# Performance work log

Hardware: AMD Instinct MI355X
Metric: run time of the kernel (lower is better)

The kernel has to match this reference:

```python
import jax, jax.numpy as jnp
import numpy as np

B, T, D, H, TW = 4, 2048, 2048, 8, 4
DH = D // H


def setup_inputs() -> dict:
    key = jax.random.key(0)
    ks = jax.random.split(key, 16)
    s = lambda k, shape, std: jax.random.normal(k, shape, dtype=jnp.float32) * std
    inp = {
        "x": jax.random.normal(ks[0], (B, T, D), dtype=jnp.float32),
        "segment_pos": jnp.tile(jnp.arange(T, dtype=jnp.int32), (B, 1)),
        # linear_y / linear_x: width -> lru_width, std = 1/sqrt(width)
        "Wy": s(ks[1], (D, D), (1.0 / D) ** 0.5),
        "by": jnp.zeros((D,), jnp.float32),
        "Wx": s(ks[2], (D, D), (1.0 / D) ** 0.5),
        "bx": jnp.zeros((D,), jnp.float32),
        # depthwise causal conv: [temporal_width, lru_width]
        "conv_w": s(ks[3], (TW, D), (1.0 / TW) ** 0.5),
        "conv_b": jnp.zeros((D,), jnp.float32),
        # RG-LRU block-diagonal gates: [H, D/H, D/H]
        "gx_w": s(ks[4], (H, DH, DH), (1.0 / DH) ** 0.5),
        "gx_b": jnp.zeros((H, DH), jnp.float32),
        "ga_w": s(ks[5], (H, DH, DH), (1.0 / DH) ** 0.5),
        "ga_b": jnp.zeros((H, DH), jnp.float32),
        # a_param: softplus(a_param) > 0 controls decay rate
        "a_param": jnp.log(jnp.exp(jax.random.uniform(ks[6], (D,), minval=0.3, maxval=0.9)) - 1.0 + 1e-6),
        # linear_out: lru_width -> width, std = 1/sqrt(lru_width)
        "Wout": s(ks[7], (D, D), (1.0 / D) ** 0.5),
        "bout": jnp.zeros((D,), jnp.float32),
    }
    return inp


def _causal_conv1d(x, w, b, segment_pos):
    # depthwise causal conv over time; contributions from other segments masked
    t = x.shape[1]
    acc = jnp.zeros_like(x)
    for i in range(TW):
        shift = TW - 1 - i  # input at t - shift, weighted by w[i]
        xs = x if shift == 0 else jnp.pad(x, ((0, 0), (shift, 0), (0, 0)))[:, :t]
        mask = (segment_pos >= shift)[..., None].astype(x.dtype)
        acc = acc + xs * mask * w[i]
    return acc + b


def _rg_lru(x, segment_pos, gx_w, gx_b, ga_w, ga_b, a_param):
    b, t, d = x.shape
    xr = x.reshape(b, t, H, DH)
    gate_x = jax.nn.sigmoid(jnp.einsum("bthi,hij->bthj", xr, gx_w) + gx_b).reshape(b, t, d)
    gate_a = jax.nn.sigmoid(jnp.einsum("bthi,hij->bthj", xr, ga_w) + ga_b).reshape(b, t, d)
    log_a = -8.0 * gate_a * jax.nn.softplus(a_param)  # [B,T,D]
    a = jnp.exp(log_a)
    reset = (segment_pos == 0)[..., None]  # [B,T,1]
    multiplier = jnp.sqrt(jnp.maximum(1.0 - jnp.exp(2.0 * log_a), 0.0))
    multiplier = jnp.where(reset, 1.0, multiplier)
    normed = x * gate_x * multiplier
    a_scan = jnp.where(reset, 0.0, a)

    def step(h, inputs):
        a_t, x_t = inputs
        h = a_t * h + x_t
        return h, h

    h0 = jnp.zeros((b, d), x.dtype)
    _, ys = jax.lax.scan(step, h0, (a_scan.transpose(1, 0, 2), normed.transpose(1, 0, 2)))
    return ys.transpose(1, 0, 2)


def reference(x, segment_pos, Wy, by, Wx, bx, conv_w, conv_b, gx_w, gx_b, ga_w, ga_b, a_param, Wout, bout):
    y = jax.nn.gelu(x @ Wy.T + by, approximate=True)
    x_proj = x @ Wx.T + bx
    x_conv = _causal_conv1d(x_proj, conv_w, conv_b, segment_pos)
    x_lru = _rg_lru(x_conv, segment_pos, gx_w, gx_b, ga_w, ga_b, a_param)
    out = (x_lru * y) @ Wout.T + bout
    return out
```

## Files before the change

kernel.cpp:

```cpp
#include <hip/hip_runtime.h>
#include <cstdint>
#include <cstddef>

typedef __bf16 bf16;
typedef __bf16 bf16x8 __attribute__((ext_vector_type(8)));
typedef float f32x4 __attribute__((ext_vector_type(4)));

#define BDIM 4
#define TDIM 2048
#define DDIM 2048
#define HDIM 8
#define DHD 256
#define MTOT 8192
#define NCHUNK 64
#define LCHUNK 32

__device__ __forceinline__ void stage16(const bf16* g, bf16* l) {
  __builtin_amdgcn_global_load_lds(
      (const __attribute__((address_space(1))) void*)g,
      (__attribute__((address_space(3))) void*)l, 16, 0, 0);
}

#define SBAR() asm volatile("s_barrier" ::: "memory")
#define WAITVM(N) asm volatile("s_waitcnt vmcnt(" #N ")" ::: "memory")

__device__ __forceinline__ float sigmoid_f(float x) {
  return __fdividef(1.f, 1.f + __expf(-x));
}
__device__ __forceinline__ float gelu_tanh(float v) {
  float u = 0.7978845608028654f * (v + 0.044715f * v * v * v);
  u = fminf(fmaxf(u, -15.f), 15.f);
  float t = __expf(2.f * u);
  return 0.5f * v * (1.f + __fdividef(t - 1.f, t + 1.f));
}
__device__ __forceinline__ float softplus_f(float x) {
  return __logf(1.f + __expf(x));
}

__global__ __launch_bounds__(256) void f2b(const float* __restrict__ src,
                                           bf16* __restrict__ dst) {
  size_t i = ((size_t)blockIdx.x * 256 + threadIdx.x) * 8;
  const float4 a = *(const float4*)(src + i);
  const float4 b = *(const float4*)(src + i + 4);
  bf16x8 r;
  r[0] = (bf16)a.x; r[1] = (bf16)a.y; r[2] = (bf16)a.z; r[3] = (bf16)a.w;
  r[4] = (bf16)b.x; r[5] = (bf16)b.y; r[6] = (bf16)b.z; r[7] = (bf16)b.w;
  *(bf16x8*)(dst + i) = r;
}

template <typename TO, int EPI>
__global__ __launch_bounds__(512, 2) void gemm256(
    const bf16* __restrict__ A, const bf16* __restrict__ Bm,
    const float* __restrict__ bias, TO* __restrict__ C,
    int K, int lda, int ldb, int ldc) {
  const int n0 = blockIdx.x * 256;
  const int m0 = blockIdx.y * 256;
  __shared__ bf16 sA[2][256][64];
  __shared__ bf16 sB[2][256][64];
  const int tid = threadIdx.x;
  const int lane = tid & 63;
  const int wid = tid >> 6;
  const int wr = wid >> 2;
  const int wc = wid & 3;
  const int quad = lane >> 4;
  const int l15 = lane & 15;

  const int sr = tid >> 3;
  const int ks8 = ((tid & 7) ^ (sr & 7)) << 3;
  const bf16* Ag = A + (size_t)(m0 + sr) * lda + ks8;
  const bf16* Bg = Bm + (size_t)(n0 + sr) * ldb + ks8;

  const int swz0 = ((quad) ^ (l15 & 7)) << 3;
  const int swz1 = ((4 + quad) ^ (l15 & 7)) << 3;

  f32x4 acc[8][4];
#pragma unroll
  for (int i = 0; i < 8; ++i)
#pragma unroll
    for (int j = 0; j < 4; ++j)
#pragma unroll
      for (int r = 0; r < 4; ++r) acc[i][j][r] = 0.f;

  const int NT = K >> 6;

  auto STAGE = [&](int p, int tk) {
    const size_t ko = (size_t)tk << 6;
#pragma unroll
    for (int c = 0; c < 4; ++c) {
      stage16(Ag + (size_t)(c * 64) * lda + ko, &sA[p][c * 64 + wid * 8][0]);
      stage16(Bg + (size_t)(c * 64) * ldb + ko, &sB[p][c * 64 + wid * 8][0]);
    }
  };

  STAGE(0, 0);
  STAGE(1, 1);
  WAITVM(8);
  SBAR();

  int p = 0;
  for (int t = 0; t < NT; ++t) {
    const bf16* As0 = &sA[p][0][0];
    const bf16* Bs0 = &sB[p][0][0];
#pragma unroll
    for (int mh = 0; mh < 2; ++mh) {
      bf16x8 afr[4][2];
#pragma unroll
      for (int mi = 0; mi < 4; ++mi) {
        const int arow = wr * 128 + mh * 64 + mi * 16 + l15;
        afr[mi][0] = *(const bf16x8*)(As0 + arow * 64 + swz0);
        afr[mi][1] = *(const bf16x8*)(As0 + arow * 64 + swz1);
      }
#pragma unroll
      for (int nh = 0; nh < 2; ++nh) {
        bf16x8 bfr[2][2];
#pragma unroll
        for (int ni = 0; ni < 2; ++ni) {
          const int brow = wc * 64 + nh * 32 + ni * 16 + l15;
          bfr[ni][0] = *(const bf16x8*)(Bs0 + brow * 64 + swz0);
          bfr[ni][1] = *(const bf16x8*)(Bs0 + brow * 64 + swz1);
        }
        __builtin_amdgcn_s_setprio(1);
#pragma unroll
        for (int mi = 0; mi < 4; ++mi)
#pragma unroll
          for (int ni = 0; ni < 2; ++ni) {
            acc[mh * 4 + mi][nh * 2 + ni] = __builtin_amdgcn_mfma_f32_16x16x32_bf16(
                afr[mi][0], bfr[ni][0], acc[mh * 4 + mi][nh * 2 + ni], 0, 0, 0);
            acc[mh * 4 + mi][nh * 2 + ni] = __builtin_amdgcn_mfma_f32_16x16x32_bf16(
                afr[mi][1], bfr[ni][1], acc[mh * 4 + mi][nh * 2 + ni], 0, 0, 0);
          }
        __builtin_amdgcn_s_setprio(0);
      }
    }
    SBAR();
    if (t + 2 < NT) {
      STAGE(p, t + 2);
      WAITVM(8);
    } else {
      WAITVM(0);
    }
    SBAR();
    p ^= 1;
  }

#pragma unroll
  for (int nn = 0; nn < 4; ++nn) {
    const int n = n0 + wc * 64 + nn * 16 + l15;
    const float bv = bias[n];
#pragma unroll
    for (int mm = 0; mm < 8; ++mm) {
#pragma unroll
      for (int r = 0; r < 4; ++r) {
        const int m = m0 + wr * 128 + mm * 16 + quad * 4 + r;
        float v = acc[mm][nn][r] + bv;
        if (EPI == 1) v = gelu_tanh(v);
        C[(size_t)m * ldc + n] = (TO)v;
      }
    }
  }
}

__global__ __launch_bounds__(256) void gate_gemm(
    const bf16* __restrict__ xconv,
    const bf16* __restrict__ gxT, const bf16* __restrict__ gaT,
    bf16* __restrict__ gxr, bf16* __restrict__ gar) {
  const int h = blockIdx.z >> 1;
  const int g = blockIdx.z & 1;
  const bf16* A = xconv + h * DHD;
  const bf16* Bm = (g ? gaT : gxT) + (size_t)h * DHD * DHD;
  bf16* C = (g ? gar : gxr) + h * DHD;
  const int n0 = blockIdx.x * 128;
  const int m0 = blockIdx.y * 128;
  __shared__ bf16 As[128 * 32];
  __shared__ bf16 Bs[128 * 32];
  const int tid = threadIdx.x;
  const int lane = tid & 63;
  const int wid = tid >> 6;
  const int waveM = wid >> 1, waveN = wid & 1;
  const int quad = lane >> 4;
  const int l15 = lane & 15;
  const int srow = lane >> 2;
  const int scol = (lane & 3) * 8;

  f32x4 acc[4][4];
#pragma unroll
  for (int i = 0; i < 4; ++i)
#pragma unroll
    for (int j = 0; j < 4; ++j)
#pragma unroll
      for (int r = 0; r < 4; ++r) acc[i][j][r] = 0.f;

  for (int k0 = 0; k0 < DHD; k0 += 32) {
    if (k0) __syncthreads();
#pragma unroll
    for (int cc = 0; cc < 2; ++cc) {
      const int q = wid * 2 + cc;
      const int row = q * 16 + srow;
      stage16(A + (size_t)(m0 + row) * DDIM + k0 + scol, As + q * 512);
      stage16(Bm + (size_t)(n0 + row) * DHD + k0 + scol, Bs + q * 512);
    }
    __syncthreads();
    bf16x8 af[4], bfr[4];
#pragma unroll
    for (int i = 0; i < 4; ++i) {
      af[i]  = *(const bf16x8*)&As[(waveM * 64 + i * 16 + l15) * 32 + quad * 8];
      bfr[i] = *(const bf16x8*)&Bs[(waveN * 64 + i * 16 + l15) * 32 + quad * 8];
    }
#pragma unroll
    for (int i = 0; i < 4; ++i)
#pragma unroll
      for (int j = 0; j < 4; ++j)
        acc[i][j] = __builtin_amdgcn_mfma_f32_16x16x32_bf16(af[i], bfr[j], acc[i][j], 0, 0, 0);
  }

#pragma unroll
  for (int j = 0; j < 4; ++j) {
    const int n = n0 + waveN * 64 + j * 16 + l15;
#pragma unroll
    for (int i = 0; i < 4; ++i) {
#pragma unroll
      for (int r = 0; r < 4; ++r) {
        const int m = m0 + waveM * 64 + i * 16 + quad * 4 + r;
        C[(size_t)m * DDIM + n] = (bf16)acc[i][j][r];
      }
    }
  }
}

__global__ __launch_bounds__(256) void conv_kernel(
    const bf16* __restrict__ xp, const float* __restrict__ cw,
    const float* __restrict__ cb, const int* __restrict__ segp,
    bf16* __restrict__ xc) {
  int v = blockIdx.x * 256 + threadIdx.x;
  int dv = v & (DDIM / 8 - 1);
  int m = v >> 8;
  int d0 = dv * 8;
  int t = m & (TDIM - 1);
  int sp = segp[m];
  float acc[8];
#pragma unroll
  for (int j = 0; j < 8; ++j) acc[j] = cb[d0 + j];
#pragma unroll
  for (int i = 0; i < 4; ++i) {
    int shift = 3 - i;
    if (t >= shift && sp >= shift) {
      bf16x8 xv = *(const bf16x8*)&xp[(size_t)(m - shift) * DDIM + d0];
#pragma unroll
      for (int j = 0; j < 8; ++j) acc[j] = fmaf((float)xv[j], cw[i * DDIM + d0 + j], acc[j]);
    }
  }
  bf16x8 o;
#pragma unroll
  for (int j = 0; j < 8; ++j) o[j] = (bf16)acc[j];
  *(bf16x8*)&xc[(size_t)m * DDIM + d0] = o;
}

__global__ __launch_bounds__(256) void transpose_gates(
    const float* __restrict__ gxw, const float* __restrict__ gaw,
    bf16* __restrict__ gxT, bf16* __restrict__ gaT) {
  __shared__ bf16 tile[32][33];
  int zz = blockIdx.z;
  int h = zz >> 1;
  const float* src = (zz & 1) ? gaw : gxw;
  bf16* dst = (zz & 1) ? gaT : gxT;
  int j0 = blockIdx.x * 32;
  int i0 = blockIdx.y * 32;
  int r = threadIdx.x >> 5;
  int c = threadIdx.x & 31;
  for (int rr = r; rr < 32; rr += 8)
    tile[rr][c] = (bf16)src[(size_t)(h * DHD + i0 + rr) * DHD + j0 + c];
  __syncthreads();
  for (int rr = r; rr < 32; rr += 8)
    dst[(size_t)(h * DHD + j0 + rr) * DHD + i0 + c] = tile[c][rr];
}

__device__ __forceinline__ void lru_elem(float pgx, float pga, float xc,
                                         float spv, bool reset,
                                         float& a, float& nr) {
  const float gx = sigmoid_f(pgx);
  const float ga = sigmoid_f(pga);
  const float la = -8.f * ga * spv;
  a = reset ? 0.f : __expf(la);
  const float mult = reset ? 1.f : sqrtf(fmaxf(1.f - __expf(2.f * la), 0.f));
  nr = xc * gx * mult;
}

__global__ __launch_bounds__(256) void scan_phase1(
    const bf16* __restrict__ gxr, const bf16* __restrict__ gar,
    const bf16* __restrict__ xconv,
    const float* __restrict__ gxb, const float* __restrict__ gab,
    const float* __restrict__ apar, const int* __restrict__ segp,
    float* __restrict__ chA, float* __restrict__ chH) {
  int idx = blockIdx.x * 256 + threadIdx.x;
  int d = idx & (DDIM - 1);
  int c = (idx >> 11) & (NCHUNK - 1);
  int b = idx >> 17;
  const float gxbv = gxb[d], gabv = gab[d];
  const float spv = softplus_f(apar[d]);
  const int mrow = b * TDIM + c * LCHUNK;
  size_t base = (size_t)mrow * DDIM + d;
  float A = 1.f, hh = 0.f;
  for (int i = 0; i < LCHUNK; ++i) {
    size_t o = base + (size_t)i * DDIM;
    float a, nr;
    lru_elem((float)gxr[o] + gxbv, (float)gar[o] + gabv, (float)xconv[o],
             spv, segp[mrow + i] == 0, a, nr);
    hh = fmaf(a, hh, nr);
    A *= a;
  }
  int ci = (b * NCHUNK + c) * DDIM + d;
  chA[ci] = A;
  chH[ci] = hh;
}

__global__ __launch_bounds__(256) void scan_phase2(
    const float* __restrict__ chA, const float* __restrict__ chH,
    float* __restrict__ hst) {
  int idx = blockIdx.x * 256 + threadIdx.x;
  int d = idx & (DDIM - 1);
  int b = idx >> 11;
  float s = 0.f;
  for (int c = 0; c < NCHUNK; ++c) {
    int ci = (b * NCHUNK + c) * DDIM + d;
    hst[ci] = s;
    s = fmaf(chA[ci], s, chH[ci]);
  }
}

__global__ __launch_bounds__(256) void scan_phase3(
    const bf16* __restrict__ gxr, const bf16* __restrict__ gar,
    const bf16* __restrict__ xconv,
    const float* __restrict__ gxb, const float* __restrict__ gab,
    const float* __restrict__ apar, const int* __restrict__ segp,
    const float* __restrict__ hst, bf16* __restrict__ yz) {
  int idx = blockIdx.x * 256 + threadIdx.x;
  int d = idx & (DDIM - 1);
  int c = (idx >> 11) & (NCHUNK - 1);
  int b = idx >> 17;
  const float gxbv = gxb[d], gabv = gab[d];
  const float spv = softplus_f(apar[d]);
  const int mrow = b * TDIM + c * LCHUNK;
  size_t base = (size_t)mrow * DDIM + d;
  float hh = hst[(b * NCHUNK + c) * DDIM + d];
  for (int i = 0; i < LCHUNK; ++i) {
    size_t o = base + (size_t)i * DDIM;
    float a, nr;
    lru_elem((float)gxr[o] + gxbv, (float)gar[o] + gabv, (float)xconv[o],
             spv, segp[mrow + i] == 0, a, nr);
    hh = fmaf(a, hh, nr);
    yz[o] = (bf16)(hh * (float)yz[o]);
  }
}

extern "C" void kernel_launch(void* const* d_in, const int* in_sizes, int n_in,
                              void* d_out, int out_size, void* d_ws, size_t ws_size,
                              hipStream_t stream) {
  const float* x    = (const float*)d_in[0];
  const int*   segp = (const int*)d_in[1];
  const float* Wy   = (const float*)d_in[2];
  const float* by   = (const float*)d_in[3];
  const float* Wx   = (const float*)d_in[4];
  const float* bx   = (const float*)d_in[5];
  const float* cw   = (const float*)d_in[6];
  const float* cb   = (const float*)d_in[7];
  const float* gxw  = (const float*)d_in[8];
  const float* gxb  = (const float*)d_in[9];
  const float* gaw  = (const float*)d_in[10];
  const float* gab  = (const float*)d_in[11];
  const float* apar = (const float*)d_in[12];
  const float* Wout = (const float*)d_in[13];
  const float* bout = (const float*)d_in[14];

  const size_t MD = (size_t)MTOT * DDIM;
  const size_t WD = (size_t)DDIM * DDIM;
  bf16* xb    = (bf16*)d_out;
  bf16* xproj = (bf16*)((char*)d_out + MD * 2);
  bf16* xconv = xb;
  bf16* gxr   = xproj;

  char* ws = (char*)d_ws;
  bf16*  gar = (bf16*)ws;
  bf16*  W1  = (bf16*)(ws + MD * 2);
  bf16*  WB1 = (bf16*)(ws + 2 * MD * 2);
  bf16*  WB2 = (bf16*)(ws + 2 * MD * 2 + WD * 2);
  char*  tail = ws + 2 * MD * 2 + 2 * WD * 2;
  const size_t GW = (size_t)HDIM * DHD * DHD * 2;
  const size_t CH = (size_t)BDIM * NCHUNK * DDIM * 4;
  bf16*  gxT = (bf16*)tail;
  bf16*  gaT = (bf16*)(tail + GW);
  float* chA = (float*)(tail + 2 * GW);
  float* chH = (float*)(tail + 2 * GW + CH);
  float* hst = (float*)(tail + 2 * GW + 2 * CH);

  dim3 blk(256);
  f2b<<<dim3(MD / 2048), blk, 0, stream>>>(x, xb);
  f2b<<<dim3(WD / 2048), blk, 0, stream>>>(Wx, WB1);
  f2b<<<dim3(WD / 2048), blk, 0, stream>>>(Wy, WB2);
  transpose_gates<<<dim3(8, 8, 16), blk, 0, stream>>>(gxw, gaw, gxT, gaT);

  gemm256<bf16, 0><<<dim3(8, 32), dim3(512), 0, stream>>>(xb, WB1, bx, xproj, DDIM, DDIM, DDIM, DDIM);
  gemm256<bf16, 1><<<dim3(8, 32), dim3(512), 0, stream>>>(xb, WB2, by, W1, DDIM, DDIM, DDIM, DDIM);

  conv_kernel<<<dim3(MTOT * (DDIM / 8) / 256), blk, 0, stream>>>(xproj, cw, cb, segp, xconv);

  gate_gemm<<<dim3(2, 64, 16), blk, 0, stream>>>(xconv, gxT, gaT, gxr, gar);

  scan_phase1<<<dim3(BDIM * NCHUNK * DDIM / 256), blk, 0, stream>>>(
      gxr, gar, xconv, gxb, gab, apar, segp, chA, chH);
  scan_phase2<<<dim3(BDIM * DDIM / 256), blk, 0, stream>>>(chA, chH, hst);
  scan_phase3<<<dim3(BDIM * NCHUNK * DDIM / 256), blk, 0, stream>>>(
      gxr, gar, xconv, gxb, gab, apar, segp, hst, W1);

  f2b<<<dim3(WD / 2048), blk, 0, stream>>>(Wout, WB1);
  gemm256<float, 0><<<dim3(8, 32), dim3(512), 0, stream>>>(W1, WB1, bout, (float*)d_out, DDIM, DDIM, DDIM, DDIM);
}
```

Before: 452.4 us.

## Interleave LDS reads, global staging and MFMA clusters in GEMM main loop; remap workgroups

Restructures the GEMM main loop into four MFMA quadrants, with LDS fragment reads and global-to-LDS staging of the next tile spread between them under extra barriers, so memory traffic overlaps with matrix math. The loop-end wait-and-barrier pair becomes a single wait at the top of each iteration. It also remaps workgroup IDs in chunks of eight, intended to improve L2/XCD locality across the grid. In exchange there are more barriers per iteration and higher register pressure from holding all A and B fragments. The early overwrite of the current buffer relies on every fragment already having been read into registers.

Measured after the change: 420.5 us. 7.1% less time.

```diff
diff --git a/kernel.cpp b/kernel.cpp
--- a/kernel.cpp
+++ b/kernel.cpp
@@ -23,6 +23,7 @@
 
 #define SBAR() asm volatile("s_barrier" ::: "memory")
 #define WAITVM(N) asm volatile("s_waitcnt vmcnt(" #N ")" ::: "memory")
+#define LGKM0() asm volatile("s_waitcnt lgkmcnt(0)" ::: "memory")
 
 __device__ __forceinline__ float sigmoid_f(float x) {
   return __fdividef(1.f, 1.f + __expf(-x));
@@ -53,8 +54,14 @@
     const bf16* __restrict__ A, const bf16* __restrict__ Bm,
     const float* __restrict__ bias, TO* __restrict__ C,
     int K, int lda, int ldb, int ldc) {
-  const int n0 = blockIdx.x * 256;
-  const int m0 = blockIdx.y * 256;
+  const int gx = gridDim.x, gy = gridDim.y;
+  const int nwg = gx * gy;
+  const int did = blockIdx.x + gx * blockIdx.y;
+  const int cpx = nwg >> 3;
+  const int lid = (did & 7) * cpx + (did >> 3);
+  const int n0 = (lid % gx) * 256;
+  const int m0 = (lid / gx) * 256;
+
   __shared__ bf16 sA[2][256][64];
   __shared__ bf16 sB[2][256][64];
   const int tid = threadIdx.x;
@@ -83,65 +90,88 @@
 
   const int NT = K >> 6;
 
-  auto STAGE = [&](int p, int tk) {
-    const size_t ko = (size_t)tk << 6;
-#pragma unroll
-    for (int c = 0; c < 4; ++c) {
-      stage16(Ag + (size_t)(c * 64) * lda + ko, &sA[p][c * 64 + wid * 8][0]);
-      stage16(Bg + (size_t)(c * 64) * ldb + ko, &sB[p][c * 64 + wid * 8][0]);
-    }
-  };
-
-  STAGE(0, 0);
-  STAGE(1, 1);
-  WAITVM(8);
-  SBAR();
+#define STAGE_A(P, TK)                                                        \
+  do {                                                                        \
+    const size_t ko_ = (size_t)(TK) << 6;                                     \
+    _Pragma("unroll") for (int c_ = 0; c_ < 4; ++c_)                          \
+        stage16(Ag + (size_t)(c_ * 64) * lda + ko_,                           \
+                &sA[P][c_ * 64 + wid * 8][0]);                                \
+  } while (0)
+#define STAGE_B(P, TK)                                                        \
+  do {                                                                        \
+    const size_t ko_ = (size_t)(TK) << 6;                                     \
+    _Pragma("unroll") for (int c_ = 0; c_ < 4; ++c_)                          \
+        stage16(Bg + (size_t)(c_ * 64) * ldb + ko_,                           \
+                &sB[P][c_ * 64 + wid * 8][0]);                                \
+  } while (0)
+
+  bf16x8 afr[2][4][2], bfr[2][2][2];
+
+#define READ_A(MH)                                                            \
+  do {                                                                        \
+    _Pragma("unroll") for (int mi_ = 0; mi_ < 4; ++mi_) {                     \
+      const int arow_ = wr * 128 + (MH) * 64 + mi_ * 16 + l15;                \
+      afr[MH][mi_][0] = *(const bf16x8*)(As0 + arow_ * 64 + swz0);            \
+      afr[MH][mi_][1] = *(const bf16x8*)(As0 + arow_ * 64 + swz1);            \
+    }                                                                         \
+  } while (0)
+#define READ_B(NH)                                                            \
+  do {                                                                        \
+    _Pragma("unroll") for (int ni_ = 0; ni_ < 2; ++ni_) {                     \
+      const int brow_ = wc * 64 + (NH) * 32 + ni_ * 16 + l15;                 \
+      bfr[NH][ni_][0] = *(const bf16x8*)(Bs0 + brow_ * 64 + swz0);            \
+      bfr[NH][ni_][1] = *(const bf16x8*)(Bs0 + brow_ * 64 + swz1);            \
+    }                                                                         \
+  } while (0)
+#define MFMA_QUAD(MH, NH)                                                     \
+  do {                                                                        \
+    __builtin_amdgcn_s_setprio(1);                                            \
+    _Pragma("unroll") for (int mi_ = 0; mi_ < 4; ++mi_)                       \
+        _Pragma("unroll") for (int ni_ = 0; ni_ < 2; ++ni_) {                 \
+      acc[(MH)*4 + mi_][(NH)*2 + ni_] = __builtin_amdgcn_mfma_f32_16x16x32_bf16( \
+          afr[MH][mi_][0], bfr[NH][ni_][0], acc[(MH)*4 + mi_][(NH)*2 + ni_], 0, 0, 0); \
+      acc[(MH)*4 + mi_][(NH)*2 + ni_] = __builtin_amdgcn_mfma_f32_16x16x32_bf16( \
+          afr[MH][mi_][1], bfr[NH][ni_][1], acc[(MH)*4 + mi_][(NH)*2 + ni_], 0, 0, 0); \
+    }                                                                         \
+    __builtin_amdgcn_s_setprio(0);                                            \
+  } while (0)
+
+  STAGE_A(0, 0);
+  STAGE_B(0, 0);
+  STAGE_A(1, 1);
+  STAGE_B(1, 1);
 
   int p = 0;
   for (int t = 0; t < NT; ++t) {
+    if (t == NT - 1) { WAITVM(0); } else { WAITVM(8); }
+    SBAR();
     const bf16* As0 = &sA[p][0][0];
     const bf16* Bs0 = &sB[p][0][0];
-#pragma unroll
-    for (int mh = 0; mh < 2; ++mh) {
-      bf16x8 afr[4][2];
-#pragma unroll
-      for (int mi = 0; mi < 4; ++mi) {
-        const int arow = wr * 128 + mh * 64 + mi * 16 + l15;
-        afr[mi][0] = *(const bf16x8*)(As0 + arow * 64 + swz0);
-        afr[mi][1] = *(const bf16x8*)(As0 + arow * 64 + swz1);
-      }
-#pragma unroll
-      for (int nh = 0; nh < 2; ++nh) {
-        bf16x8 bfr[2][2];
-#pragma unroll
-        for (int ni = 0; ni < 2; ++ni) {
-          const int brow = wc * 64 + nh * 32 + ni * 16 + l15;
-          bfr[ni][0] = *(const bf16x8*)(Bs0 + brow * 64 + swz0);
-          bfr[ni][1] = *(const bf16x8*)(Bs0 + brow * 64 + swz1);
-        }
-        __builtin_amdgcn_s_setprio(1);
-#pragma unroll
-        for (int mi = 0; mi < 4; ++mi)
-#pragma unroll
-          for (int ni = 0; ni < 2; ++ni) {
-            acc[mh * 4 + mi][nh * 2 + ni] = __builtin_amdgcn_mfma_f32_16x16x32_bf16(
-                afr[mi][0], bfr[ni][0], acc[mh * 4 + mi][nh * 2 + ni], 0, 0, 0);
-            acc[mh * 4 + mi][nh * 2 + ni] = __builtin_amdgcn_mfma_f32_16x16x32_bf16(
-                afr[mi][1], bfr[ni][1], acc[mh * 4 + mi][nh * 2 + ni], 0, 0, 0);
-          }
-        __builtin_amdgcn_s_setprio(0);
-      }
-    }
-    SBAR();
-    if (t + 2 < NT) {
-      STAGE(p, t + 2);
-      WAITVM(8);
-    } else {
-      WAITVM(0);
-    }
-    SBAR();
+    READ_A(0);
+    READ_B(0);
+    SBAR();
+    MFMA_QUAD(0, 0);
+    SBAR();
+    READ_A(1);
+    READ_B(1);
+    LGKM0();
+    __builtin_amdgcn_sched_barrier(0);
+    SBAR();
+    MFMA_QUAD(0, 1);
+    SBAR();
+    if (t + 2 < NT) STAGE_A(p, t + 2);
+    MFMA_QUAD(1, 0);
+    SBAR();
+    if (t + 2 < NT) STAGE_B(p, t + 2);
+    MFMA_QUAD(1, 1);
     p ^= 1;
   }
+
+#undef STAGE_A
+#undef STAGE_B
+#undef READ_A
+#undef READ_B
+#undef MFMA_QUAD
 
 #pragma unroll
   for (int nn = 0; nn < 4; ++nn) {
```
